# Optimization experiments

Measured on AMD Instinct MI355X. Metric: run time of the kernel, lower is better.

Reference implementation:

```python
import jax, jax.numpy as jnp
import numpy as np

D_MODEL = 1024
KEY_MODEL = 1024
D_K = 64
D_V = 64
N_HEAD = 8
PROJ = N_HEAD * D_V  # 512


def setup_inputs() -> dict:
    key = jax.random.key(0)
    ks = jax.random.split(key, 9)
    N, M = 8192, 8192
    s = 0.02
    return {
        "q": jax.random.normal(ks[0], (N, D_MODEL), jnp.float32),
        "k": jax.random.normal(ks[1], (M, KEY_MODEL), jnp.float32),
        "v": jax.random.normal(ks[2], (M, D_MODEL), jnp.float32),
        "Wq": jax.random.normal(ks[3], (D_MODEL, PROJ), jnp.float32) * s,
        "bq": jnp.zeros((PROJ,), jnp.float32),
        "Wk": jax.random.normal(ks[4], (KEY_MODEL, PROJ), jnp.float32) * s,
        "bk": jnp.zeros((PROJ,), jnp.float32),
        "Wv": jax.random.normal(ks[5], (D_MODEL, PROJ), jnp.float32) * s,
        "bv": jnp.zeros((PROJ,), jnp.float32),
    }


def reference(q, k, v, Wq, bq, Wk, bk, Wv, bv):
    # Linear projections (torch nn.Linear: x @ W^T + b; here W stored as [in,out])
    qp = q @ Wq + bq                      # [N, PROJ]
    kp = k @ Wk + bk                      # [M, PROJ]
    vp = v @ Wv + bv                      # [M, PROJ]
    # Note: original scales by d_k (NOT sqrt(d_k)); dropout is identity at eval.
    scores = (qp @ kp.T) / D_K            # [N, M]
    attn = jax.nn.softmax(scores, axis=-1)
    return attn @ vp                      # [N, PROJ]
```

## Files before the change

### kernel.cpp

```cpp
#include <hip/hip_runtime.h>
#include <hip/hip_bf16.h>
#include <stdint.h>
#include <stddef.h>

typedef unsigned short u16;
typedef short bf16x8 __attribute__((ext_vector_type(8)));
typedef float floatx4 __attribute__((ext_vector_type(4)));

#define N_ROWS 8192
#define D_MODEL 1024
#define PROJ 512
#define MHALF 4096
#define SCALE_LOG2E_DK 0.022542110013890054f

#define VMCNT_WAIT(n) asm volatile("s_waitcnt vmcnt(" #n ")" ::: "memory")

__device__ __forceinline__ float bf2f(u16 u) {
    union { unsigned int i; float f; } x; x.i = ((unsigned int)u) << 16; return x.f;
}
__device__ __forceinline__ u16 f2bf(float f) {
    __hip_bfloat16 h = __float2bfloat16(f);
    return *reinterpret_cast<u16*>(&h);
}

__device__ __forceinline__ void gload_lds16(u16* lds_base, const u16* g) {
    __builtin_amdgcn_global_load_lds(
        (const __attribute__((address_space(1))) void*)g,
        (__attribute__((address_space(3))) void*)lds_base,
        16, 0, 0);
}

__device__ __forceinline__ void stage128x32(u16* lds, const u16* src, int stride,
                                            int wv, int ln) {
    const int rr = ln >> 2;
    const int cc = (ln & 3) << 3;
#pragma unroll
    for (int i = 0; i < 2; ++i) {
        const int rb = i * 64 + wv * 16;
        gload_lds16(lds + rb * 32, src + (size_t)(rb + rr) * stride + cc);
    }
}

__global__ void transpose_w_kernel(const float* __restrict__ in, u16* __restrict__ out,
                                   int R, int C) {
    __shared__ u16 tile[32][33];
    int r = blockIdx.y * 32 + threadIdx.y;
    int c = blockIdx.x * 32 + threadIdx.x;
    tile[threadIdx.y][threadIdx.x] = f2bf(in[(size_t)r * C + c]);
    __syncthreads();
    int ro = blockIdx.x * 32 + threadIdx.y;
    int co = blockIdx.y * 32 + threadIdx.x;
    out[(size_t)ro * R + co] = tile[threadIdx.x][threadIdx.y];
}

__global__ void transpose_kernel(const u16* __restrict__ in, u16* __restrict__ out,
                                 int R, int C) {
    __shared__ u16 tile[32][33];
    int r = blockIdx.y * 32 + threadIdx.y;
    int c = blockIdx.x * 32 + threadIdx.x;
    tile[threadIdx.y][threadIdx.x] = in[(size_t)r * C + c];
    __syncthreads();
    int ro = blockIdx.x * 32 + threadIdx.y;
    int co = blockIdx.y * 32 + threadIdx.x;
    out[(size_t)ro * R + co] = tile[threadIdx.x][threadIdx.y];
}

__global__ __launch_bounds__(256) void convert_bf16_kernel(
    const float* __restrict__ q, const float* __restrict__ k, const float* __restrict__ v,
    u16* __restrict__ qb, u16* __restrict__ kb, u16* __restrict__ vb)
{
    const float* in = (blockIdx.y == 0) ? q : (blockIdx.y == 1) ? k : v;
    u16* out        = (blockIdx.y == 0) ? qb : (blockIdx.y == 1) ? kb : vb;
    size_t i = ((size_t)blockIdx.x * 256 + threadIdx.x) * 8;
    float4 a = *(const float4*)(in + i);
    float4 b = *(const float4*)(in + i + 4);
    bf16x8 o;
    o[0] = (short)f2bf(a.x); o[1] = (short)f2bf(a.y);
    o[2] = (short)f2bf(a.z); o[3] = (short)f2bf(a.w);
    o[4] = (short)f2bf(b.x); o[5] = (short)f2bf(b.y);
    o[6] = (short)f2bf(b.z); o[7] = (short)f2bf(b.w);
    *(bf16x8*)(out + i) = o;
}

__global__ __launch_bounds__(256) void proj_kernel(
    const u16* __restrict__ qb, const u16* __restrict__ kb, const u16* __restrict__ vb,
    const u16* __restrict__ WqT, const u16* __restrict__ WkT, const u16* __restrict__ WvT,
    const float* __restrict__ bq, const float* __restrict__ bk, const float* __restrict__ bv,
    u16* __restrict__ qp, u16* __restrict__ kp, u16* __restrict__ vp)
{
    const int z = blockIdx.z;
    const u16* A      = (z == 0) ? qb  : (z == 1) ? kb  : vb;
    const u16* WT     = (z == 0) ? WqT : (z == 1) ? WkT : WvT;
    const float* bias = (z == 0) ? bq  : (z == 1) ? bk  : bv;
    u16* C            = (z == 0) ? qp  : (z == 1) ? kp  : vp;

    const int m0 = blockIdx.x * 128;
    const int n0 = blockIdx.y * 128;
    __shared__ __align__(16) u16 smem[2 * 128 * 32];
    u16* As = smem;
    u16* Bs = smem + 128 * 32;

    const int t = threadIdx.x;
    const int wv = t >> 6, ln = t & 63;
    const int q16 = ln >> 4, l16 = ln & 15;
    const int wm = (wv & 1) * 64, wn = (wv >> 1) * 64;

    floatx4 acc[4][4] = {};

    for (int k0 = 0; k0 < D_MODEL; k0 += 32) {
        __syncthreads();
        stage128x32(As, A  + (size_t)m0 * D_MODEL + k0, D_MODEL, wv, ln);
        stage128x32(Bs, WT + (size_t)n0 * D_MODEL + k0, D_MODEL, wv, ln);
        __syncthreads();

        bf16x8 af[4], bfr[4];
#pragma unroll
        for (int mi = 0; mi < 4; ++mi)
            af[mi] = *(const bf16x8*)(As + (wm + mi * 16 + l16) * 32 + q16 * 8);
#pragma unroll
        for (int ni = 0; ni < 4; ++ni)
            bfr[ni] = *(const bf16x8*)(Bs + (wn + ni * 16 + l16) * 32 + q16 * 8);
#pragma unroll
        for (int mi = 0; mi < 4; ++mi)
#pragma unroll
            for (int ni = 0; ni < 4; ++ni)
                acc[mi][ni] = __builtin_amdgcn_mfma_f32_16x16x32_bf16(
                    af[mi], bfr[ni], acc[mi][ni], 0, 0, 0);
    }

#pragma unroll
    for (int ni = 0; ni < 4; ++ni) {
        int col = n0 + wn + ni * 16 + l16;
        float bv_ = bias[col];
#pragma unroll
        for (int mi = 0; mi < 4; ++mi)
#pragma unroll
            for (int rr = 0; rr < 4; ++rr) {
                int row = m0 + wm + mi * 16 + q16 * 4 + rr;
                C[(size_t)row * PROJ + col] = f2bf(acc[mi][ni][rr] + bv_);
            }
    }
}

__global__ void zero_l_kernel(float* __restrict__ l) {
    l[blockIdx.x * 256 + threadIdx.x] = 0.f;
}

__global__ __launch_bounds__(256) void score_kernel(
    const u16* __restrict__ qp, const u16* __restrict__ kph,
    u16* __restrict__ P, float* __restrict__ l)
{
    const int m0 = blockIdx.x * 128;
    const int n0 = blockIdx.y * 128;
    __shared__ __align__(16) u16 smem[2 * 128 * 32];
    u16* As = smem;
    u16* Bs = smem + 128 * 32;

    const int t = threadIdx.x;
    const int wv = t >> 6, ln = t & 63;
    const int q16 = ln >> 4, l16 = ln & 15;
    const int wm = (wv & 1) * 64, wn = (wv >> 1) * 64;

    floatx4 acc[4][4] = {};

    for (int k0 = 0; k0 < PROJ; k0 += 32) {
        __syncthreads();
        stage128x32(As, qp  + (size_t)m0 * PROJ + k0, PROJ, wv, ln);
        stage128x32(Bs, kph + (size_t)n0 * PROJ + k0, PROJ, wv, ln);
        __syncthreads();

        bf16x8 af[4], bfr[4];
#pragma unroll
        for (int mi = 0; mi < 4; ++mi)
            af[mi] = *(const bf16x8*)(As + (wm + mi * 16 + l16) * 32 + q16 * 8);
#pragma unroll
        for (int ni = 0; ni < 4; ++ni)
            bfr[ni] = *(const bf16x8*)(Bs + (wn + ni * 16 + l16) * 32 + q16 * 8);
#pragma unroll
        for (int mi = 0; mi < 4; ++mi)
#pragma unroll
            for (int ni = 0; ni < 4; ++ni)
                acc[mi][ni] = __builtin_amdgcn_mfma_f32_16x16x32_bf16(
                    af[mi], bfr[ni], acc[mi][ni], 0, 0, 0);
    }

#pragma unroll
    for (int mi = 0; mi < 4; ++mi)
#pragma unroll
        for (int rr = 0; rr < 4; ++rr) {
            int row = m0 + wm + mi * 16 + q16 * 4 + rr;
            u16* Prow = P + (size_t)row * MHALF + n0 + wn;
            float tot = 0.f;
#pragma unroll
            for (int ni = 0; ni < 4; ++ni) {
                float x = acc[mi][ni][rr] * SCALE_LOG2E_DK;
                x = fminf(fmaxf(x, -30.f), 30.f);
                float p = exp2f(x);
                tot += p;
                Prow[ni * 16 + l16] = f2bf(p);
            }
#pragma unroll
            for (int m = 1; m < 16; m <<= 1)
                tot += __shfl_xor(tot, m, 64);
            if (l16 == 0)
                atomicAdd(&l[row], tot);
        }
}

__global__ __launch_bounds__(256) void pv_kernel(
    const u16* __restrict__ P, const u16* __restrict__ vpTh,
    float* __restrict__ Ofull, u16* __restrict__ Opart, int accum)
{
    const int m0 = blockIdx.x * 128;
    const int n0 = blockIdx.y * 128;
    const int kg = blockIdx.z;
    const int kbase = kg * 2048;
    __shared__ __align__(16) u16 smem[4 * 8192];

    const int t = threadIdx.x;
    const int wv = t >> 6, ln = t & 63;
    const int q16 = ln >> 4, l16 = ln & 15;
    const int wm = (wv & 1) * 64, wn = (wv >> 1) * 64;

    const u16* Abase = P    + (size_t)m0 * MHALF  + kbase;
    const u16* Bbase = vpTh + (size_t)n0 * N_ROWS + kbase;

    floatx4 acc[4][4] = {};

    auto STAGE = [&](int ti) {
        u16* buf = smem + (ti & 3) * 8192;
        stage128x32(buf,        Abase + ti * 32, MHALF,  wv, ln);
        stage128x32(buf + 4096, Bbase + ti * 32, N_ROWS, wv, ln);
    };
    auto COMPUTE = [&](int ti) {
        const u16* As = smem + (ti & 3) * 8192;
        const u16* Bs = As + 4096;
        bf16x8 af[4], bfr[4];
#pragma unroll
        for (int mi = 0; mi < 4; ++mi)
            af[mi] = *(const bf16x8*)(As + (wm + mi * 16 + l16) * 32 + q16 * 8);
#pragma unroll
        for (int ni = 0; ni < 4; ++ni)
            bfr[ni] = *(const bf16x8*)(Bs + (wn + ni * 16 + l16) * 32 + q16 * 8);
#pragma unroll
        for (int mi = 0; mi < 4; ++mi)
#pragma unroll
            for (int ni = 0; ni < 4; ++ni)
                acc[mi][ni] = __builtin_amdgcn_mfma_f32_16x16x32_bf16(
                    af[mi], bfr[ni], acc[mi][ni], 0, 0, 0);
    };

    const int NT = 2048 / 32;
    STAGE(0); STAGE(1); STAGE(2);

    for (int ti = 0; ti < NT - 2; ++ti) {
        VMCNT_WAIT(8);
        __builtin_amdgcn_sched_barrier(0);
        __builtin_amdgcn_s_barrier();
        __builtin_amdgcn_sched_barrier(0);
        if (ti + 3 < NT) STAGE(ti + 3);
        COMPUTE(ti);
    }
    VMCNT_WAIT(4);
    __builtin_amdgcn_sched_barrier(0);
    __builtin_amdgcn_s_barrier();
    __builtin_amdgcn_sched_barrier(0);
    COMPUTE(NT - 2);
    VMCNT_WAIT(0);
    __builtin_amdgcn_sched_barrier(0);
    __builtin_amdgcn_s_barrier();
    __builtin_amdgcn_sched_barrier(0);
    COMPUTE(NT - 1);

#pragma unroll
    for (int ni = 0; ni < 4; ++ni) {
        int col = n0 + wn + ni * 16 + l16;
#pragma unroll
        for (int mi = 0; mi < 4; ++mi)
#pragma unroll
            for (int rr = 0; rr < 4; ++rr) {
                int row = m0 + wm + mi * 16 + q16 * 4 + rr;
                size_t o = (size_t)row * PROJ + col;
                float v = acc[mi][ni][rr];
                if (kg == 0) {
                    if (accum) v += Ofull[o];
                    Ofull[o] = v;
                } else {
                    if (accum) v += bf2f(Opart[o]);
                    Opart[o] = f2bf(v);
                }
            }
    }
}

__global__ void scale_kernel(float* __restrict__ out, const u16* __restrict__ Opart,
                             const float* __restrict__ l)
{
    int idx = blockIdx.x * 256 + threadIdx.x;
    int row = idx >> 9;
    out[idx] = (out[idx] + bf2f(Opart[idx])) / l[row];
}

extern "C" void kernel_launch(void* const* d_in, const int* in_sizes, int n_in,
                              void* d_out, int out_size, void* d_ws, size_t ws_size,
                              hipStream_t stream)
{
    (void)in_sizes; (void)n_in; (void)out_size;
    if (ws_size < ((size_t)101 << 20)) return;

    const float* q  = (const float*)d_in[0];
    const float* k  = (const float*)d_in[1];
    const float* v  = (const float*)d_in[2];
    const float* Wq = (const float*)d_in[3];
    const float* bq = (const float*)d_in[4];
    const float* Wk = (const float*)d_in[5];
    const float* bk = (const float*)d_in[6];
    const float* Wv = (const float*)d_in[7];
    const float* bv = (const float*)d_in[8];

    char* ws = (char*)d_ws;
    u16* qp    = (u16*)(ws);
    u16* kp    = (u16*)(ws + ((size_t)8  << 20));
    u16* vp    = (u16*)(ws + ((size_t)16 << 20));
    u16* vpT   = (u16*)(ws + ((size_t)24 << 20));
    u16* WqT   = (u16*)(ws + ((size_t)32 << 20));
    u16* WkT   = (u16*)(ws + ((size_t)33 << 20));
    u16* WvT   = (u16*)(ws + ((size_t)34 << 20));
    float* l   = (float*)(ws + ((size_t)35 << 20));
    u16* P     = (u16*)(ws + ((size_t)36 << 20));
    u16* qb    = (u16*)(ws + ((size_t)36 << 20));
    u16* kb    = (u16*)(ws + ((size_t)52 << 20));
    u16* vb    = (u16*)(ws + ((size_t)68 << 20));
    u16* Opart = vp;
    float* Ofull = (float*)d_out;

    dim3 tb(32, 32);
    transpose_w_kernel<<<dim3(16, 32), tb, 0, stream>>>(Wq, WqT, 1024, 512);
    transpose_w_kernel<<<dim3(16, 32), tb, 0, stream>>>(Wk, WkT, 1024, 512);
    transpose_w_kernel<<<dim3(16, 32), tb, 0, stream>>>(Wv, WvT, 1024, 512);

    convert_bf16_kernel<<<dim3(4096, 3), 256, 0, stream>>>(q, k, v, qb, kb, vb);

    proj_kernel<<<dim3(64, 4, 3), 256, 0, stream>>>(qb, kb, vb, WqT, WkT, WvT,
                                                    bq, bk, bv, qp, kp, vp);

    transpose_kernel<<<dim3(16, 256), tb, 0, stream>>>(vp, vpT, 8192, 512);

    zero_l_kernel<<<32, 256, 0, stream>>>(l);

    score_kernel<<<dim3(64, 32), 256, 0, stream>>>(qp, kp, P, l);
    pv_kernel<<<dim3(64, 4, 2), 256, 0, stream>>>(P, vpT, Ofull, Opart, 0);
    score_kernel<<<dim3(64, 32), 256, 0, stream>>>(qp, kp + (size_t)MHALF * PROJ, P, l);
    pv_kernel<<<dim3(64, 4, 2), 256, 0, stream>>>(P, vpT + MHALF, Ofull, Opart, 1);

    scale_kernel<<<16384, 256, 0, stream>>>(Ofull, Opart, l);
}
```

Before: 407.7 us.

## Pipeline GEMM tile staging with 4-deep shared-memory ring in proj and score kernels

Replaces the synchronous load-then-compute loop in the projection and score GEMMs with a 4-buffer LDS ring that prefetches three K-tiles ahead. It uses explicit vmcnt waits and a single barrier per iteration, so global loads overlap with MFMA compute and one of the two barriers per tile is dropped. In exchange, LDS use per block grows to 64KB, which can lower occupancy. Correctness depends on stage128x32 issuing direct-to-LDS loads whose counts match the vmcnt thresholds.

```diff
diff --git a/kernel.cpp b/kernel.cpp
--- a/kernel.cpp
+++ b/kernel.cpp
@@ -96,23 +96,26 @@
 
     const int m0 = blockIdx.x * 128;
     const int n0 = blockIdx.y * 128;
-    __shared__ __align__(16) u16 smem[2 * 128 * 32];
-    u16* As = smem;
-    u16* Bs = smem + 128 * 32;
+    __shared__ __align__(16) u16 smem[4 * 8192];
 
     const int t = threadIdx.x;
     const int wv = t >> 6, ln = t & 63;
     const int q16 = ln >> 4, l16 = ln & 15;
     const int wm = (wv & 1) * 64, wn = (wv >> 1) * 64;
 
+    const u16* Abase = A  + (size_t)m0 * D_MODEL;
+    const u16* Bbase = WT + (size_t)n0 * D_MODEL;
+
     floatx4 acc[4][4] = {};
 
-    for (int k0 = 0; k0 < D_MODEL; k0 += 32) {
-        __syncthreads();
-        stage128x32(As, A  + (size_t)m0 * D_MODEL + k0, D_MODEL, wv, ln);
-        stage128x32(Bs, WT + (size_t)n0 * D_MODEL + k0, D_MODEL, wv, ln);
-        __syncthreads();
-
+    auto STAGE = [&](int ti) {
+        u16* buf = smem + (ti & 3) * 8192;
+        stage128x32(buf,        Abase + ti * 32, D_MODEL, wv, ln);
+        stage128x32(buf + 4096, Bbase + ti * 32, D_MODEL, wv, ln);
+    };
+    auto COMPUTE = [&](int ti) {
+        const u16* As = smem + (ti & 3) * 8192;
+        const u16* Bs = As + 4096;
         bf16x8 af[4], bfr[4];
 #pragma unroll
         for (int mi = 0; mi < 4; ++mi)
@@ -126,7 +129,28 @@
             for (int ni = 0; ni < 4; ++ni)
                 acc[mi][ni] = __builtin_amdgcn_mfma_f32_16x16x32_bf16(
                     af[mi], bfr[ni], acc[mi][ni], 0, 0, 0);
-    }
+    };
+
+    const int NT = D_MODEL / 32;
+    STAGE(0); STAGE(1); STAGE(2);
+    for (int ti = 0; ti < NT - 2; ++ti) {
+        VMCNT_WAIT(8);
+        __builtin_amdgcn_sched_barrier(0);
+        __builtin_amdgcn_s_barrier();
+        __builtin_amdgcn_sched_barrier(0);
+        if (ti + 3 < NT) STAGE(ti + 3);
+        COMPUTE(ti);
+    }
+    VMCNT_WAIT(4);
+    __builtin_amdgcn_sched_barrier(0);
+    __builtin_amdgcn_s_barrier();
+    __builtin_amdgcn_sched_barrier(0);
+    COMPUTE(NT - 2);
+    VMCNT_WAIT(0);
+    __builtin_amdgcn_sched_barrier(0);
+    __builtin_amdgcn_s_barrier();
+    __builtin_amdgcn_sched_barrier(0);
+    COMPUTE(NT - 1);
 
 #pragma unroll
     for (int ni = 0; ni < 4; ++ni) {
@@ -152,23 +176,26 @@
 {
     const int m0 = blockIdx.x * 128;
     const int n0 = blockIdx.y * 128;
-    __shared__ __align__(16) u16 smem[2 * 128 * 32];
-    u16* As = smem;
-    u16* Bs = smem + 128 * 32;
+    __shared__ __align__(16) u16 smem[4 * 8192];
 
     const int t = threadIdx.x;
     const int wv = t >> 6, ln = t & 63;
     const int q16 = ln >> 4, l16 = ln & 15;
     const int wm = (wv & 1) * 64, wn = (wv >> 1) * 64;
 
+    const u16* Abase = qp  + (size_t)m0 * PROJ;
+    const u16* Bbase = kph + (size_t)n0 * PROJ;
+
     floatx4 acc[4][4] = {};
 
-    for (int k0 = 0; k0 < PROJ; k0 += 32) {
-        __syncthreads();
-        stage128x32(As, qp  + (size_t)m0 * PROJ + k0, PROJ, wv, ln);
-        stage128x32(Bs, kph + (size_t)n0 * PROJ + k0, PROJ, wv, ln);
-        __syncthreads();
-
+    auto STAGE = [&](int ti) {
+        u16* buf = smem + (ti & 3) * 8192;
+        stage128x32(buf,        Abase + ti * 32, PROJ, wv, ln);
+        stage128x32(buf + 4096, Bbase + ti * 32, PROJ, wv, ln);
+    };
+    auto COMPUTE = [&](int ti) {
+        const u16* As = smem + (ti & 3) * 8192;
+        const u16* Bs = As + 4096;
         bf16x8 af[4], bfr[4];
 #pragma unroll
         for (int mi = 0; mi < 4; ++mi)
@@ -182,7 +209,28 @@
             for (int ni = 0; ni < 4; ++ni)
                 acc[mi][ni] = __builtin_amdgcn_mfma_f32_16x16x32_bf16(
                     af[mi], bfr[ni], acc[mi][ni], 0, 0, 0);
-    }
+    };
+
+    const int NT = PROJ / 32;
+    STAGE(0); STAGE(1); STAGE(2);
+    for (int ti = 0; ti < NT - 2; ++ti) {
+        VMCNT_WAIT(8);
+        __builtin_amdgcn_sched_barrier(0);
+        __builtin_amdgcn_s_barrier();
+        __builtin_amdgcn_sched_barrier(0);
+        if (ti + 3 < NT) STAGE(ti + 3);
+        COMPUTE(ti);
+    }
+    VMCNT_WAIT(4);
+    __builtin_amdgcn_sched_barrier(0);
+    __builtin_amdgcn_s_barrier();
+    __builtin_amdgcn_sched_barrier(0);
+    COMPUTE(NT - 2);
+    VMCNT_WAIT(0);
+    __builtin_amdgcn_sched_barrier(0);
+    __builtin_amdgcn_s_barrier();
+    __builtin_amdgcn_sched_barrier(0);
+    COMPUTE(NT - 1);
 
 #pragma unroll
     for (int mi = 0; mi < 4; ++mi)
```

After: 423.2 us. 1.04x slower.
